# Kernel tuning notes

Measured on AMD Instinct MI355X. Metric: run time of the kernel, lower is better.

## Reference

```python
import jax, jax.numpy as jnp
import numpy as np

WS = 7        # window size
MAXD = 3      # correlation max displacement -> (2*3+1)^2 = 49 channels
T = 8         # hardcoded temporal length in forward
NUM_HEADS = 8


def setup_inputs() -> dict:
    key = jax.random.key(0)
    ks = jax.random.split(key, 5)
    B, H, W, C = 2, 56, 56, 128
    N = T * H * W
    x = jax.random.normal(ks[0], (B, N, C), jnp.float32)
    qkv_w = jax.random.normal(ks[1], (3 * C, C), jnp.float32) * 0.02
    proj_w = jax.random.normal(ks[2], (C, C), jnp.float32) * 0.02
    proj_b = jnp.zeros((C,), jnp.float32)
    pos_embed1 = jax.random.normal(ks[3], (1, WS * WS, 49), jnp.float32) * 0.02
    pos_embed2 = jax.random.normal(ks[4], (1, WS * WS, C // NUM_HEADS), jnp.float32) * 0.02
    return dict(x=x, qkv_w=qkv_w, proj_w=proj_w, proj_b=proj_b,
                pos_embed1=pos_embed1, pos_embed2=pos_embed2)


def _l2norm(x, axis):
    return x / jnp.maximum(jnp.sqrt(jnp.sum(x * x, axis=axis, keepdims=True)), 1e-12)


def _correlation(a, b):
    # a, b: (B, C, H, W) -> (B, H, W, 49); zero-padded shifted dot products over C
    Bc, Cc, H, W = a.shape
    bp = jnp.pad(b, ((0, 0), (0, 0), (MAXD, MAXD), (MAXD, MAXD)))
    outs = [jnp.sum(a * bp[:, :, du:du + H, dv:dv + W], axis=1)
            for du in range(2 * MAXD + 1) for dv in range(2 * MAXD + 1)]
    return jnp.stack(outs, axis=-1)


def _windows(x):
    # x: (B, H, W, D) -> (B*nh*nw, WS*WS, D); H split as (WS, nh) per torch reshape
    Bc, H, W, D = x.shape
    nh, nw = H // WS, W // WS
    x = x.reshape(Bc, WS, nh, WS, nw, D).transpose(0, 2, 4, 1, 3, 5)
    return x.reshape(Bc * nh * nw, WS * WS, D)


def _unwindows(x, Bc, H, W):
    nh, nw = H // WS, W // WS
    D = x.shape[-1]
    x = x.reshape(Bc, nh, nw, WS, WS, D).transpose(0, 3, 1, 4, 2, 5)
    return x.reshape(Bc, H, W, D)


def reference(x, qkv_w, proj_w, proj_b, pos_embed1, pos_embed2):
    B, N, C = x.shape
    H = int(np.sqrt(N // T)); W = H
    hd = C // NUM_HEADS
    BT = B * NUM_HEADS * T

    qkv = (x @ qkv_w.T).reshape(B, N, 3, NUM_HEADS, hd).transpose(2, 0, 3, 1, 4)
    q, k, v = qkv[0], qkv[1], qkv[2]            # (B, heads, N, hd)

    q = q.reshape(B * NUM_HEADS, T, H, W, hd).transpose(0, 1, 4, 2, 3)  # (B*h, T, hd, H, W)
    k = k.reshape(B * NUM_HEADS, T, H, W, hd).transpose(0, 1, 4, 2, 3)
    v = v.reshape(BT, H * W, hd)

    k_post = jnp.concatenate([k[:, 1:], k[:, -1:]], axis=1)  # shift by one frame
    qp = _l2norm(q.reshape(BT, hd, H, W), axis=1)
    kp = _l2norm(k_post.reshape(BT, hd, H, W), axis=1)

    corr = _correlation(qp, kp)                 # (BT, H, W, 49)
    corr = _windows(corr) + pos_embed1          # (BT*nh*nw, 49, 49)
    motion_attn = jax.nn.softmax(jnp.einsum('bnd,bmd->bnm', corr, corr), axis=-1)

    motion_v = _windows(v.reshape(BT, H, W, hd))
    motion_x = _unwindows(motion_attn @ motion_v, BT, H, W)

    qw = _windows(qp.transpose(0, 2, 3, 1)) + pos_embed2
    app_attn = jax.nn.softmax(jnp.einsum('bnd,bmd->bnm', qw, qw), axis=-1)
    app_x = _unwindows(app_attn @ motion_v, BT, H, W)

    out = 0.5 * app_x + 0.5 * motion_x          # (BT, H, W, hd)
    out = out.reshape(B, NUM_HEADS, T, H, W, hd).transpose(0, 2, 3, 4, 1, 5).reshape(B, N, C)
    return out @ proj_w.T + proj_b
```

## Files before the change

### kernel.cpp

```cpp
#include <hip/hip_runtime.h>
#include <math.h>

constexpr int H_   = 56;
constexpr int HW_  = 56 * 56;
constexpr int NPIX = 8 * HW_;
constexpr int SLAB = 128 * HW_ * 16;
constexpr int CWST = 52;

typedef __attribute__((ext_vector_type(8))) short bf16x8;
typedef __attribute__((ext_vector_type(4))) float f32x4;
typedef __attribute__((ext_vector_type(4))) unsigned int u32x4;

__device__ __forceinline__ unsigned short f2bf(float x) {
  unsigned int u = __float_as_uint(x);
  unsigned int r = (u + 0x7fffu + ((u >> 16) & 1u)) >> 16;
  return (unsigned short)r;
}
__device__ __forceinline__ float bf2f(unsigned short h) {
  return __uint_as_float(((unsigned int)h) << 16);
}

template <int MODE>
__global__ __launch_bounds__(256, 3) void gemm128(
    const float* X, const float* __restrict__ Wt, const float* __restrict__ bias,
    float* __restrict__ Yq, float* __restrict__ Yk, float* __restrict__ Yv,
    float* Yout)
{
  __shared__ float xT[32][132];
  __shared__ float wT[32][132];
  const int tid = threadIdx.x;
  const int tx = tid & 15, ty = tid >> 4;
  const int mbase = blockIdx.x * 128;
  const int nt = (MODE == 0) ? (int)blockIdx.y : 0;
  const float* Wp = Wt + (size_t)nt * (128 * 128);

  float acc[8][8];
#pragma unroll
  for (int i = 0; i < 8; ++i)
#pragma unroll
    for (int j = 0; j < 8; ++j) acc[i][j] = 0.f;

  const int srow = tid >> 3;
  const int scol = (tid & 7) * 4;

  for (int kt = 0; kt < 4; ++kt) {
    if (kt) __syncthreads();
#pragma unroll
    for (int p = 0; p < 4; ++p) {
      int r = p * 32 + srow;
      float4 vx = *(const float4*)&X [(size_t)(mbase + r) * 128 + kt * 32 + scol];
      float4 vw = *(const float4*)&Wp[(size_t)r * 128 + kt * 32 + scol];
      xT[scol + 0][r] = vx.x; xT[scol + 1][r] = vx.y; xT[scol + 2][r] = vx.z; xT[scol + 3][r] = vx.w;
      wT[scol + 0][r] = vw.x; wT[scol + 1][r] = vw.y; wT[scol + 2][r] = vw.z; wT[scol + 3][r] = vw.w;
    }
    __syncthreads();
#pragma unroll 4
    for (int c = 0; c < 32; ++c) {
      float4 a0 = *(const float4*)&xT[c][tx * 4];
      float4 a1 = *(const float4*)&xT[c][64 + tx * 4];
      float4 b0 = *(const float4*)&wT[c][ty * 4];
      float4 b1 = *(const float4*)&wT[c][64 + ty * 4];
      float a[8] = {a0.x, a0.y, a0.z, a0.w, a1.x, a1.y, a1.z, a1.w};
      float b[8] = {b0.x, b0.y, b0.z, b0.w, b1.x, b1.y, b1.z, b1.w};
#pragma unroll
      for (int i = 0; i < 8; ++i)
#pragma unroll
        for (int j = 0; j < 8; ++j) acc[i][j] += a[i] * b[j];
    }
  }

  if (MODE == 0) {
    const int hq = ty >> 2;
    const int cq = (ty & 3) * 4;
    float* Ybase = (nt == 0) ? Yq : ((nt == 1) ? Yk : Yv);
#pragma unroll
    for (int i = 0; i < 8; ++i) {
      int gpix = mbase + ((i < 4) ? (tx * 4 + i) : (64 + tx * 4 + (i - 4)));
      int b = gpix / NPIX;
      int rem = gpix - b * NPIX;
      int t = rem / HW_;
      int s = rem - t * HW_;
      float s0 = acc[i][0]*acc[i][0] + acc[i][1]*acc[i][1] + acc[i][2]*acc[i][2] + acc[i][3]*acc[i][3];
      float s1 = acc[i][4]*acc[i][4] + acc[i][5]*acc[i][5] + acc[i][6]*acc[i][6] + acc[i][7]*acc[i][7];
      s0 += __shfl_xor(s0, 16); s0 += __shfl_xor(s0, 32);
      s1 += __shfl_xor(s1, 16); s1 += __shfl_xor(s1, 32);
      float r0 = 1.f, r1 = 1.f;
      if (nt < 2) {
        r0 = 1.f / fmaxf(sqrtf(s0), 1e-12f);
        r1 = 1.f / fmaxf(sqrtf(s1), 1e-12f);
      }
      int bt0 = (b * 8 + hq) * 8 + t;
      int bt1 = (b * 8 + hq + 4) * 8 + t;
      float* d0 = Ybase + ((size_t)bt0 * HW_ + s) * 16 + cq;
      float* d1 = Ybase + ((size_t)bt1 * HW_ + s) * 16 + cq;
      *(float4*)d0 = make_float4(acc[i][0]*r0, acc[i][1]*r0, acc[i][2]*r0, acc[i][3]*r0);
      *(float4*)d1 = make_float4(acc[i][4]*r1, acc[i][5]*r1, acc[i][6]*r1, acc[i][7]*r1);
    }
  } else {
    float4 bb0 = *(const float4*)&bias[ty * 4];
    float4 bb1 = *(const float4*)&bias[64 + ty * 4];
#pragma unroll
    for (int i = 0; i < 8; ++i) {
      int gpix = mbase + ((i < 4) ? (tx * 4 + i) : (64 + tx * 4 + (i - 4)));
      float* dst = Yout + (size_t)gpix * 128;
      *(float4*)&dst[ty * 4]      = make_float4(acc[i][0]+bb0.x, acc[i][1]+bb0.y, acc[i][2]+bb0.z, acc[i][3]+bb0.w);
      *(float4*)&dst[64 + ty * 4] = make_float4(acc[i][4]+bb1.x, acc[i][5]+bb1.y, acc[i][6]+bb1.z, acc[i][7]+bb1.w);
    }
  }
}

__global__ __launch_bounds__(256) void corr_dense(
    const float* __restrict__ qn, const float* __restrict__ kn,
    const float* __restrict__ pos1,
    unsigned int* __restrict__ cwpk, float* __restrict__ diib)
{
  __shared__ float kS[10 * 1120];
  const int bid = blockIdx.x;
  const int xcd = bid & 7;
  const int j = bid >> 3;
  const int g = j / 14;
  const int strip = j - g * 14;
  const int bt = xcd * 16 + g;
  const int h0 = strip * 4;
  const int t = bt & 7;
  const int btk = bt - t + ((t < 7) ? (t + 1) : 7);
  const float* qb = qn + (size_t)bt  * (HW_ * 16);
  const float* kb = kn + (size_t)btk * (HW_ * 16);
  const int tid = threadIdx.x;

  for (int idx = tid; idx < 2240; idx += 256) {
    int r = idx / 224;
    int c = idx - r * 224;
    int hh = h0 - 3 + r;
    f32x4 v = (f32x4)0.f;
    if ((unsigned)hh < 56u)
      v = *(const f32x4*)(kb + (size_t)(hh * 56) * 16 + c * 4);
    *(f32x4*)&kS[r * 1120 + (c >> 2) * 20 + (c & 3) * 4] = v;
  }
  __syncthreads();

  if (tid < 224) {
    const int py = tid / 56;
    const int h = h0 + py;
    const int w = tid - py * 56;
    const f32x4* qp = (const f32x4*)(qb + (size_t)(h * 56 + w) * 16);
    f32x4 q0 = qp[0], q1 = qp[1], q2 = qp[2], q3 = qp[3];
    const int ridx = (h >> 3) * 7 + (w >> 3);
    const float* p1r = pos1 + ridx * 49;
    unsigned int* outr = cwpk + (size_t)(bt * HW_ + h * 56 + w) * CWST;
    float dii = 0.f;
#pragma unroll
    for (int d4 = 0; d4 < 12; ++d4) {
      f32x4 kv[4][4];
#pragma unroll
      for (int e = 0; e < 4; ++e) {
        const int d = d4 * 4 + e;
        const int du = d / 7, dv = d % 7;
        const int ww = w + dv - 3;
        const int wc = ww < 0 ? 0 : (ww > 55 ? 55 : ww);
        const float* kp = &kS[(py + du) * 1120 + wc * 20];
        kv[e][0] = *(const f32x4*)kp;
        kv[e][1] = *(const f32x4*)(kp + 4);
        kv[e][2] = *(const f32x4*)(kp + 8);
        kv[e][3] = *(const f32x4*)(kp + 12);
      }
      unsigned int pk[4];
#pragma unroll
      for (int e = 0; e < 4; ++e) {
        const int d = d4 * 4 + e;
        const int dv = d % 7;
        const int ww = w + dv - 3;
        f32x4 a4 = q0 * kv[e][0] + q1 * kv[e][1] + q2 * kv[e][2] + q3 * kv[e][3];
        float pd = (a4.x + a4.y) + (a4.z + a4.w);
        pd = ((unsigned)ww < 56u) ? pd : 0.f;
        const float val = pd + p1r[d];
        dii += val * val;
        unsigned short hb = f2bf(val);
        unsigned short lb = f2bf(val - bf2f(hb));
        pk[e] = (unsigned)hb | ((unsigned)lb << 16);
      }
      *(u32x4*)(outr + d4 * 4) = *(const u32x4*)pk;
    }
    {
      const int ww = w + 3;
      const int wc = ww > 55 ? 55 : ww;
      const float* kp = &kS[(py + 6) * 1120 + wc * 20];
      f32x4 k0 = *(const f32x4*)kp;
      f32x4 k1 = *(const f32x4*)(kp + 4);
      f32x4 k2 = *(const f32x4*)(kp + 8);
      f32x4 k3 = *(const f32x4*)(kp + 12);
      f32x4 a4 = q0 * k0 + q1 * k1 + q2 * k2 + q3 * k3;
      float pd = (a4.x + a4.y) + (a4.z + a4.w);
      pd = ((unsigned)ww < 56u) ? pd : 0.f;
      const float val = pd + p1r[48];
      dii += val * val;
      unsigned short hb = f2bf(val);
      unsigned short lb = f2bf(val - bf2f(hb));
      outr[48] = (unsigned)hb | ((unsigned)lb << 16);
    }
    diib[bt * HW_ + h * 56 + w] = dii;
  }
}

__global__ __launch_bounds__(64, 2) void attn_mfma(
    const float* __restrict__ qn, const float* __restrict__ vv,
    const unsigned int* __restrict__ cwpk, const float* __restrict__ diib,
    const float* __restrict__ pos2, float* __restrict__ mid)
{
  __shared__ __align__(16) unsigned char smem[7808];
  unsigned short* Pb   = (unsigned short*)smem;
  float*          mi_s = (float*)(smem + 7104);
  float*          scm  = (float*)(smem + 7300);
  float*          sca  = (float*)(smem + 7500);

  const int lane = threadIdx.x;
  const int lg = lane >> 4;
  const int lr = lane & 15;
  const int bid = blockIdx.x;
  const int xcd = bid & 7;
  const int j = bid >> 3;
  const int bt = xcd * 16 + (j >> 6);
  const int win = j & 63;
  const int wy = win >> 3;
  const int wx = win & 7;
  const float* qb = qn + (size_t)bt * (HW_ * 16);
  const float* vb = vv + (size_t)bt * (HW_ * 16);
  const unsigned int* cwb = cwpk + (size_t)bt * HW_ * CWST;
  const float* dib = diib + (size_t)bt * HW_;

  const bool rowok = (lane < 49);
  const int il = rowok ? lane : 48;

  float xv[2][8];
#pragma unroll
  for (int ks = 0; ks < 2; ++ks) {
#pragma unroll
    for (int e = 0; e < 8; ++e) {
      int k = ks * 32 + lg * 8 + e;
      int kc2 = (k < 49) ? k : 0;
      int ka = (kc2 * 37) >> 8;
      int kb2 = kc2 - ka * 7;
      float x = vb[(size_t)((ka * 8 + wy) * 56 + (kb2 * 8 + wx)) * 16 + lr];
      xv[ks][e] = (k < 49) ? x : 0.f;
    }
  }

  {
    const int ia = (il * 37) >> 8;
    const int ib = il - ia * 7;
    float dii = dib[(ia * 8 + wy) * 56 + (ib * 8 + wx)];
    float md = dii;
#pragma unroll
    for (int o = 32; o >= 1; o >>= 1) md = fmaxf(md, __shfl_xor(md, o));
    if (rowok) mi_s[il] = sqrtf(dii * md);
  }

  bf16x8 ah[4][2], al[4][2];
#pragma unroll
  for (int half = 0; half < 2; ++half) {
    u32x4 raw[2][2][2];
#pragma unroll
    for (int u = 0; u < 2; ++u) {
      const int tt2 = half * 2 + u;
      const int row = tt2 * 16 + lr;
      const int rowc = (row < 49) ? row : 0;
      const int a2 = (rowc * 37) >> 8;
      const int b3 = rowc - a2 * 7;
      const unsigned int* src = cwb + (size_t)((a2 * 8 + wy) * 56 + (b3 * 8 + wx)) * CWST;
#pragma unroll
      for (int ks = 0; ks < 2; ++ks) {
        const int cb = ks * 32 + lg * 8;
        raw[u][ks][0] = *(const u32x4*)(src + cb);
        raw[u][ks][1] = *(const u32x4*)(src + cb + 4);
      }
    }
#pragma unroll
    for (int u = 0; u < 2; ++u) {
      const int tt2 = half * 2 + u;
      const int row = tt2 * 16 + lr;
      const bool rv = (row < 49);
#pragma unroll
      for (int ks = 0; ks < 2; ++ks) {
        const int cb = ks * 32 + lg * 8;
        unsigned int u0[8];
        *(u32x4*)&u0[0] = raw[u][ks][0];
        *(u32x4*)&u0[4] = raw[u][ks][1];
#pragma unroll
        for (int e = 0; e < 8; ++e)
          if (!rv || (cb + e) >= 49) u0[e] = 0u;
        union { u32x4 uu; bf16x8 s; } Hh, Ll;
#pragma unroll
        for (int p = 0; p < 4; ++p) {
          Hh.uu[p] = (u0[2*p] & 0xffffu) | (u0[2*p+1] << 16);
          Ll.uu[p] = (u0[2*p] >> 16) | (u0[2*p+1] & 0xffff0000u);
        }
        ah[tt2][ks] = Hh.s;
        al[tt2][ks] = Ll.s;
      }
    }
  }

#pragma unroll
  for (int rt = 0; rt < 4; ++rt) {
    f32x4 C[4];
#pragma unroll
    for (int ct = 0; ct < 4; ++ct) C[ct] = (f32x4)0.f;
#pragma unroll
    for (int ks = 0; ks < 2; ++ks) {
#pragma unroll
      for (int ct = 0; ct < 4; ++ct) {
        C[ct] = __builtin_amdgcn_mfma_f32_16x16x32_bf16(ah[rt][ks], ah[ct][ks], C[ct], 0, 0, 0);
        C[ct] = __builtin_amdgcn_mfma_f32_16x16x32_bf16(ah[rt][ks], al[ct][ks], C[ct], 0, 0, 0);
        C[ct] = __builtin_amdgcn_mfma_f32_16x16x32_bf16(al[rt][ks], ah[ct][ks], C[ct], 0, 0, 0);
      }
    }
#pragma unroll
    for (int reg = 0; reg < 4; ++reg) {
      int row = rt * 16 + lg * 4 + reg;
      float m = mi_s[(row < 49) ? row : 0];
#pragma unroll
      for (int ct = 0; ct < 4; ++ct) {
        float p = __expf(C[ct][reg] - m);
        if (row < 49) Pb[row * 72 + ct * 16 + lr] = f2bf(p);
      }
    }
  }
  asm volatile("" ::: "memory");

  if (rowok) {
    const u32x4* pr = (const u32x4*)(Pb + il * 72);
    unsigned int uu[28];
#pragma unroll
    for (int w = 0; w < 7; ++w) *(u32x4*)&uu[4*w] = pr[w];
    float s = 0.f;
#pragma unroll
    for (int w = 0; w < 24; ++w)
      s += bf2f((unsigned short)(uu[w] & 0xffffu)) + bf2f((unsigned short)(uu[w] >> 16));
    s += bf2f((unsigned short)(uu[24] & 0xffffu));
    scm[il] = 0.5f / s;
  }

  bf16x8 vfh[2], vfl[2];
#pragma unroll
  for (int ks = 0; ks < 2; ++ks) {
    union { u32x4 u; bf16x8 s; } Hh, Ll;
#pragma unroll
    for (int p = 0; p < 4; ++p) {
      unsigned short h0 = f2bf(xv[ks][2*p]);
      unsigned short h1 = f2bf(xv[ks][2*p+1]);
      unsigned short l0 = f2bf(xv[ks][2*p]   - bf2f(h0));
      unsigned short l1 = f2bf(xv[ks][2*p+1] - bf2f(h1));
      Hh.u[p] = (unsigned int)h0 | ((unsigned int)h1 << 16);
      Ll.u[p] = (unsigned int)l0 | ((unsigned int)l1 << 16);
    }
    vfh[ks] = Hh.s;
    vfl[ks] = Ll.s;
  }

  f32x4 om[4];
#pragma unroll
  for (int rt = 0; rt < 4; ++rt) om[rt] = (f32x4)0.f;
#pragma unroll
  for (int ks = 0; ks < 2; ++ks) {
#pragma unroll
    for (int rt = 0; rt < 4; ++rt) {
      int row = rt * 16 + lr;
      int rowc = (row < 49) ? row : 0;
      bf16x8 pa = *(const bf16x8*)(Pb + rowc * 72 + ks * 32 + lg * 8);
      om[rt] = __builtin_amdgcn_mfma_f32_16x16x32_bf16(pa, vfh[ks], om[rt], 0, 0, 0);
      om[rt] = __builtin_amdgcn_mfma_f32_16x16x32_bf16(pa, vfl[ks], om[rt], 0, 0, 0);
    }
  }
  asm volatile("s_waitcnt lgkmcnt(0)" ::: "memory");

  bf16x8 qf[4];
#pragma unroll
  for (int half = 0; half < 2; ++half) {
    f32x4 qa_[2], qb_[2], pa_[2], pb_[2];
#pragma unroll
    for (int u = 0; u < 2; ++u) {
      const int tt2 = half * 2 + u;
      int row = tt2 * 16 + lr;
      int rowc = (row < 49) ? row : 0;
      int a2 = (rowc * 37) >> 8;
      int b3 = rowc - a2 * 7;
      const int co = (lg & 1) * 8;
      const float* qsrc = qb + (size_t)((a2 * 8 + wy) * 56 + (b3 * 8 + wx)) * 16 + co;
      qa_[u] = *(const f32x4*)qsrc;
      qb_[u] = *(const f32x4*)(qsrc + 4);
      const float* p2 = pos2 + rowc * 16 + co;
      pa_[u] = *(const f32x4*)p2;
      pb_[u] = *(const f32x4*)(p2 + 4);
    }
#pragma unroll
    for (int u = 0; u < 2; ++u) {
      const int tt2 = half * 2 + u;
      int row = tt2 * 16 + lr;
      f32x4 w0 = qa_[u] + pa_[u], w1 = qb_[u] + pb_[u];
      float ws[8] = {w0.x, w0.y, w0.z, w0.w, w1.x, w1.y, w1.z, w1.w};
      const bool zv = (row >= 49) || (lg >= 2);
      union { u32x4 u4; bf16x8 s; } Q;
#pragma unroll
      for (int p = 0; p < 4; ++p) {
        unsigned int v = (unsigned)f2bf(ws[2*p]) | ((unsigned)f2bf(ws[2*p+1]) << 16);
        Q.u4[p] = zv ? 0u : v;
      }
      qf[tt2] = Q.s;
    }
  }

#pragma unroll
  for (int rt = 0; rt < 4; ++rt) {
    f32x4 Ca[4];
#pragma unroll
    for (int ct = 0; ct < 4; ++ct) Ca[ct] = (f32x4)0.f;
#pragma unroll
    for (int ct = 0; ct < 4; ++ct)
      Ca[ct] = __builtin_amdgcn_mfma_f32_16x16x32_bf16(qf[rt], qf[ct], Ca[ct], 0, 0, 0);
#pragma unroll
    for (int reg = 0; reg < 4; ++reg) {
      int row = rt * 16 + lg * 4 + reg;
#pragma unroll
      for (int ct = 0; ct < 4; ++ct) {
        float p = __expf(Ca[ct][reg]);
        if (row < 49) Pb[row * 72 + ct * 16 + lr] = f2bf(p);
      }
    }
  }
  asm volatile("" ::: "memory");

  if (rowok) {
    const u32x4* pr = (const u32x4*)(Pb + il * 72);
    unsigned int uu[28];
#pragma unroll
    for (int w = 0; w < 7; ++w) *(u32x4*)&uu[4*w] = pr[w];
    float s = 0.f;
#pragma unroll
    for (int w = 0; w < 24; ++w)
      s += bf2f((unsigned short)(uu[w] & 0xffffu)) + bf2f((unsigned short)(uu[w] >> 16));
    s += bf2f((unsigned short)(uu[24] & 0xffffu));
    sca[il] = 0.5f / s;
  }

  f32x4 oa[4];
#pragma unroll
  for (int rt = 0; rt < 4; ++rt) oa[rt] = (f32x4)0.f;
#pragma unroll
  for (int ks = 0; ks < 2; ++ks) {
#pragma unroll
    for (int rt = 0; rt < 4; ++rt) {
      int row = rt * 16 + lr;
      int rowc = (row < 49) ? row : 0;
      bf16x8 pa = *(const bf16x8*)(Pb + rowc * 72 + ks * 32 + lg * 8);
      oa[rt] = __builtin_amdgcn_mfma_f32_16x16x32_bf16(pa, vfh[ks], oa[rt], 0, 0, 0);
      oa[rt] = __builtin_amdgcn_mfma_f32_16x16x32_bf16(pa, vfl[ks], oa[rt], 0, 0, 0);
    }
  }

  {
    int b = bt >> 6, e = (bt >> 3) & 7, tt = bt & 7;
    size_t obase = ((size_t)(b * NPIX + tt * HW_)) * 128 + e * 16 + lr;
#pragma unroll
    for (int rt = 0; rt < 4; ++rt) {
#pragma unroll
      for (int reg = 0; reg < 4; ++reg) {
        int row = rt * 16 + lg * 4 + reg;
        if (row < 49) {
          float o = om[rt][reg] * scm[row] + oa[rt][reg] * sca[row];
          int a2 = (row * 37) >> 8;
          int b3 = row - a2 * 7;
          mid[obase + (size_t)((a2 * 8 + wy) * 56 + (b3 * 8 + wx)) * 128] = o;
        }
      }
    }
  }
}

extern "C" void kernel_launch(void* const* d_in, const int* in_sizes, int n_in,
                              void* d_out, int out_size, void* d_ws, size_t ws_size,
                              hipStream_t stream) {
  (void)in_sizes; (void)n_in; (void)out_size; (void)ws_size;
  const float* x      = (const float*)d_in[0];
  const float* qkv_w  = (const float*)d_in[1];
  const float* proj_w = (const float*)d_in[2];
  const float* proj_b = (const float*)d_in[3];
  const float* pos1   = (const float*)d_in[4];
  const float* pos2   = (const float*)d_in[5];
  float* out = (float*)d_out;

  float* qn = (float*)d_ws;
  float* kc = qn + SLAB;
  float* vv = kc + SLAB;
  unsigned int* cwpk = (unsigned int*)(vv + SLAB);
  float* diib = (float*)(cwpk + (size_t)128 * HW_ * CWST + 64);

  gemm128<0><<<dim3(392, 3), 256, 0, stream>>>(x, qkv_w, nullptr, qn, kc, vv, nullptr);
  corr_dense<<<dim3(1792), 256, 0, stream>>>(qn, kc, pos1, cwpk, diib);
  attn_mfma<<<dim3(8192), 64, 0, stream>>>(qn, vv, cwpk, diib, pos2, out);
  gemm128<1><<<dim3(392), 256, 0, stream>>>(out, proj_w, proj_b, nullptr, nullptr, nullptr, out);
}
```

Baseline: 191.1 us.

## Replace FP32 QKV GEMM with split-bf16 MFMA kernel

The QKV projection now runs on a new MFMA kernel instead of the scalar FP32 tiled GEMM. Each FP32 operand is split into high and low bf16 parts, and three bf16 MFMAs per tile approximate FP32 accuracy. The per-head L2 normalisation and scatter into the head-major layout are kept in the epilogue, now reduced with lane shuffles. The aim is to move the QKV GEMM compute onto the matrix cores, at the cost of splitting the weights in-register per block and of scalar, less coalesced stores.

```diff
diff --git a/kernel.cpp b/kernel.cpp
--- a/kernel.cpp
+++ b/kernel.cpp
@@ -18,6 +18,120 @@
 }
 __device__ __forceinline__ float bf2f(unsigned short h) {
   return __uint_as_float(((unsigned int)h) << 16);
+}
+
+__global__ __launch_bounds__(256) void qkv_mfma(
+    const float* __restrict__ X, const float* __restrict__ Wt,
+    float* __restrict__ Yq, float* __restrict__ Yk, float* __restrict__ Yv)
+{
+  __shared__ unsigned int xS[128 * 68];
+  const int tid = threadIdx.x;
+  const int wave = tid >> 6, lane = tid & 63;
+  const int lg = lane >> 4, lr = lane & 15;
+  const int wm = wave >> 1, wn = wave & 1;
+  const int mbase = blockIdx.x * 128;
+  const int nt = blockIdx.y;
+  const float* Wp = Wt + (size_t)nt * (128 * 128);
+  float* Ybase = (nt == 0) ? Yq : ((nt == 1) ? Yk : Yv);
+
+  f32x4 acc[4][4];
+#pragma unroll
+  for (int mt = 0; mt < 4; ++mt)
+#pragma unroll
+    for (int ct = 0; ct < 4; ++ct) acc[mt][ct] = (f32x4)0.f;
+
+#pragma unroll
+  for (int kh = 0; kh < 2; ++kh) {
+    if (kh) __syncthreads();
+#pragma unroll
+    for (int c = 0; c < 8; ++c) {
+      const int chunk = c * 256 + tid;
+      const int row = chunk >> 4;
+      const int cc = chunk & 15;
+      f32x4 v = *(const f32x4*)(X + (size_t)(mbase + row) * 128 + kh * 64 + cc * 4);
+      unsigned int pk[4];
+#pragma unroll
+      for (int e = 0; e < 4; ++e) {
+        unsigned short hb = f2bf(v[e]);
+        unsigned short lb = f2bf(v[e] - bf2f(hb));
+        pk[e] = (unsigned)hb | ((unsigned)lb << 16);
+      }
+      *(u32x4*)&xS[row * 68 + cc * 4] = *(const u32x4*)pk;
+    }
+    __syncthreads();
+
+#pragma unroll
+    for (int ks2 = 0; ks2 < 2; ++ks2) {
+      bf16x8 ah[4], al[4];
+#pragma unroll
+      for (int mt = 0; mt < 4; ++mt) {
+        const unsigned int* s = &xS[(wm * 64 + mt * 16 + lr) * 68 + ks2 * 32 + lg * 8];
+        unsigned int u0[8];
+        *(u32x4*)&u0[0] = *(const u32x4*)s;
+        *(u32x4*)&u0[4] = *(const u32x4*)(s + 4);
+        union { u32x4 uu; bf16x8 ss; } Hh, Ll;
+#pragma unroll
+        for (int p = 0; p < 4; ++p) {
+          Hh.uu[p] = (u0[2*p] & 0xffffu) | (u0[2*p+1] << 16);
+          Ll.uu[p] = (u0[2*p] >> 16) | (u0[2*p+1] & 0xffff0000u);
+        }
+        ah[mt] = Hh.ss;
+        al[mt] = Ll.ss;
+      }
+      bf16x8 bh[4], bl[4];
+#pragma unroll
+      for (int ct = 0; ct < 4; ++ct) {
+        const float* wsrc = Wp + (size_t)(wn * 64 + ct * 16 + lr) * 128 + kh * 64 + ks2 * 32 + lg * 8;
+        f32x4 w0 = *(const f32x4*)wsrc;
+        f32x4 w1 = *(const f32x4*)(wsrc + 4);
+        float wsv[8] = {w0.x, w0.y, w0.z, w0.w, w1.x, w1.y, w1.z, w1.w};
+        union { u32x4 uu; bf16x8 ss; } Hh, Ll;
+#pragma unroll
+        for (int p = 0; p < 4; ++p) {
+          unsigned short h0 = f2bf(wsv[2*p]),     h1 = f2bf(wsv[2*p+1]);
+          unsigned short l0 = f2bf(wsv[2*p] - bf2f(h0)), l1 = f2bf(wsv[2*p+1] - bf2f(h1));
+          Hh.uu[p] = (unsigned)h0 | ((unsigned)h1 << 16);
+          Ll.uu[p] = (unsigned)l0 | ((unsigned)l1 << 16);
+        }
+        bh[ct] = Hh.ss;
+        bl[ct] = Ll.ss;
+      }
+#pragma unroll
+      for (int mt = 0; mt < 4; ++mt) {
+#pragma unroll
+        for (int ct = 0; ct < 4; ++ct) {
+          acc[mt][ct] = __builtin_amdgcn_mfma_f32_16x16x32_bf16(ah[mt], bh[ct], acc[mt][ct], 0, 0, 0);
+          acc[mt][ct] = __builtin_amdgcn_mfma_f32_16x16x32_bf16(ah[mt], bl[ct], acc[mt][ct], 0, 0, 0);
+          acc[mt][ct] = __builtin_amdgcn_mfma_f32_16x16x32_bf16(al[mt], bh[ct], acc[mt][ct], 0, 0, 0);
+        }
+      }
+    }
+  }
+
+#pragma unroll
+  for (int mt = 0; mt < 4; ++mt) {
+#pragma unroll
+    for (int reg = 0; reg < 4; ++reg) {
+      const int gpix = mbase + wm * 64 + mt * 16 + lg * 4 + reg;
+      const int b = (gpix >= NPIX) ? 1 : 0;
+      const int rem = gpix - b * NPIX;
+      const int t = rem / HW_;
+      const int sp = rem - t * HW_;
+#pragma unroll
+      for (int ct = 0; ct < 4; ++ct) {
+        float val = acc[mt][ct][reg];
+        float ss = val * val;
+        ss += __shfl_xor(ss, 1);
+        ss += __shfl_xor(ss, 2);
+        ss += __shfl_xor(ss, 4);
+        ss += __shfl_xor(ss, 8);
+        float r = 1.f;
+        if (nt < 2) r = 1.f / fmaxf(sqrtf(ss), 1e-12f);
+        const int btq = (b * 8 + wn * 4 + ct) * 8 + t;
+        Ybase[((size_t)btq * HW_ + sp) * 16 + lr] = val * r;
+      }
+    }
+  }
 }
 
 template <int MODE>
@@ -31,8 +145,7 @@
   const int tid = threadIdx.x;
   const int tx = tid & 15, ty = tid >> 4;
   const int mbase = blockIdx.x * 128;
-  const int nt = (MODE == 0) ? (int)blockIdx.y : 0;
-  const float* Wp = Wt + (size_t)nt * (128 * 128);
+  const float* Wp = Wt;
 
   float acc[8][8];
 #pragma unroll
@@ -69,34 +182,7 @@
     }
   }
 
-  if (MODE == 0) {
-    const int hq = ty >> 2;
-    const int cq = (ty & 3) * 4;
-    float* Ybase = (nt == 0) ? Yq : ((nt == 1) ? Yk : Yv);
-#pragma unroll
-    for (int i = 0; i < 8; ++i) {
-      int gpix = mbase + ((i < 4) ? (tx * 4 + i) : (64 + tx * 4 + (i - 4)));
-      int b = gpix / NPIX;
-      int rem = gpix - b * NPIX;
-      int t = rem / HW_;
-      int s = rem - t * HW_;
-      float s0 = acc[i][0]*acc[i][0] + acc[i][1]*acc[i][1] + acc[i][2]*acc[i][2] + acc[i][3]*acc[i][3];
-      float s1 = acc[i][4]*acc[i][4] + acc[i][5]*acc[i][5] + acc[i][6]*acc[i][6] + acc[i][7]*acc[i][7];
-      s0 += __shfl_xor(s0, 16); s0 += __shfl_xor(s0, 32);
-      s1 += __shfl_xor(s1, 16); s1 += __shfl_xor(s1, 32);
-      float r0 = 1.f, r1 = 1.f;
-      if (nt < 2) {
-        r0 = 1.f / fmaxf(sqrtf(s0), 1e-12f);
-        r1 = 1.f / fmaxf(sqrtf(s1), 1e-12f);
-      }
-      int bt0 = (b * 8 + hq) * 8 + t;
-      int bt1 = (b * 8 + hq + 4) * 8 + t;
-      float* d0 = Ybase + ((size_t)bt0 * HW_ + s) * 16 + cq;
-      float* d1 = Ybase + ((size_t)bt1 * HW_ + s) * 16 + cq;
-      *(float4*)d0 = make_float4(acc[i][0]*r0, acc[i][1]*r0, acc[i][2]*r0, acc[i][3]*r0);
-      *(float4*)d1 = make_float4(acc[i][4]*r1, acc[i][5]*r1, acc[i][6]*r1, acc[i][7]*r1);
-    }
-  } else {
+  {
     float4 bb0 = *(const float4*)&bias[ty * 4];
     float4 bb1 = *(const float4*)&bias[64 + ty * 4];
 #pragma unroll
@@ -494,7 +580,7 @@
   unsigned int* cwpk = (unsigned int*)(vv + SLAB);
   float* diib = (float*)(cwpk + (size_t)128 * HW_ * CWST + 64);
 
-  gemm128<0><<<dim3(392, 3), 256, 0, stream>>>(x, qkv_w, nullptr, qn, kc, vv, nullptr);
+  qkv_mfma<<<dim3(392, 3), 256, 0, stream>>>(x, qkv_w, qn, kc, vv);
   corr_dense<<<dim3(1792), 256, 0, stream>>>(qn, kc, pos1, cwpk, diib);
   attn_mfma<<<dim3(8192), 64, 0, stream>>>(qn, vv, cwpk, diib, pos2, out);
   gemm128<1><<<dim3(392), 256, 0, stream>>>(out, proj_w, proj_b, nullptr, nullptr, nullptr, out);
```

New measurement: 208.2 us. +9.0%, slower.
